# Optimization experiments

Hardware: AMD Instinct MI355X
Metric: run time of the kernel (lower is better)

## Reference

```python
import jax, jax.numpy as jnp
import numpy as np

B, T, U, V = 4, 300, 80, 1024
DE, DD, INNER = 320, 320, 512


def setup_inputs() -> dict:
    key = jax.random.key(0)
    ks = jax.random.split(key, 6)
    enc_state = jax.random.normal(ks[0], (B, T, DE), jnp.float32)
    dec_state = jax.random.normal(ks[1], (B, U + 1, DD), jnp.float32)
    Wf = jax.random.normal(ks[2], (INNER, DE + DD), jnp.float32) / np.float32(np.sqrt(DE + DD))
    bf = jnp.zeros((INNER,), jnp.float32)
    Wp = jax.random.normal(ks[3], (V, INNER), jnp.float32) / np.float32(np.sqrt(INNER))
    bp = jnp.zeros((V,), jnp.float32)
    targets = jax.random.randint(ks[4], (B, U), 1, V).astype(jnp.int32)  # labels avoid blank=0
    inputs_length = jnp.full((B,), T, jnp.int32)
    targets_length = jnp.full((B,), U, jnp.int32)
    return {"enc_state": enc_state, "dec_state": dec_state, "Wf": Wf, "bf": bf,
            "Wp": Wp, "bp": bp, "targets": targets,
            "inputs_length": inputs_length, "targets_length": targets_length}


def joint_logits(enc, dec, Wf, bf, Wp, bp):
    # Linear over concat([enc, dec]) == Linear(enc) + Linear(dec): avoids materializing the concat.
    de = enc.shape[-1]
    Wf_e, Wf_d = Wf[:, :de], Wf[:, de:]
    enc_p = jnp.einsum('btd,id->bti', enc, Wf_e)   # [B,T,inner]
    dec_p = jnp.einsum('bud,id->bui', dec, Wf_d)   # [B,U1,inner]
    h = jnp.tanh(enc_p[:, :, None, :] + dec_p[:, None, :, :] + bf)  # [B,T,U1,inner]
    return jnp.einsum('btui,vi->btuv', h, Wp) + bp  # [B,T,U1,V]


def rnnt_loss(log_probs, targets, t_len, u_len):
    # log_probs: [B,T,U1,V], blank index 0.
    lp_blank = log_probs[..., 0]  # [B,T,U1]
    lp_emit = jnp.take_along_axis(log_probs[:, :, :-1, :], targets[:, None, :, None], axis=3)[..., 0]  # [B,T,U]
    # row0: alpha[0,u] = sum_{k<u} emit[0,k]
    row0 = jnp.pad(jnp.cumsum(lp_emit[:, 0, :], axis=-1), ((0, 0), (1, 0)))  # [B,U1]

    def outer(alpha_prev, xs):
        blank_prev, emit_cur = xs  # [B,U1], [B,U]
        first = alpha_prev[:, 0] + blank_prev[:, 0]  # [B]

        def inner(c, x):
            a_plus_b, e = x  # [B],[B]
            c2 = jnp.logaddexp(a_plus_b, c + e)
            return c2, c2
        xs_in = ((alpha_prev[:, 1:] + blank_prev[:, 1:]).T, emit_cur.T)  # [U,B]
        _, rest = jax.lax.scan(inner, first, xs_in)  # [U,B]
        row = jnp.concatenate([first[None, :], rest], axis=0).T  # [B,U1]
        return row, row

    xs = (jnp.swapaxes(lp_blank[:, :-1, :], 0, 1), jnp.swapaxes(lp_emit[:, 1:, :], 0, 1))
    _, rows = jax.lax.scan(outer, row0, xs)  # [T-1,B,U1]
    alpha = jnp.concatenate([row0[None], rows], axis=0)  # [T,B,U1]
    bidx = jnp.arange(alpha.shape[1])
    ll = alpha[t_len - 1, bidx, u_len] + lp_blank[bidx, t_len - 1, u_len]
    return -jnp.mean(ll)


def reference(enc_state, dec_state, Wf, bf, Wp, bp, targets, inputs_length, targets_length):
    logits = joint_logits(enc_state, dec_state, Wf, bf, Wp, bp).astype(jnp.float32)
    log_probs = jax.nn.log_softmax(logits, axis=-1)
    return rnnt_loss(log_probs, targets, inputs_length, targets_length)
```

## Files before the change

kernel.cpp:

```cpp
#include <hip/hip_runtime.h>

#define B_DIM 4
#define T_DIM 300
#define U_DIM 80
#define UP1   81
#define V_DIM 1024
#define NINNER 512
#define NROWS (B_DIM * T_DIM * UP1)
#define EP_ROWS (B_DIM * T_DIM)
#define DP_ROWS (B_DIM * UP1)
#define NDIAG 380
#define ZSTR  168
#define ZROWS (B_DIM * NDIAG + 8)
#define WF_PART 163840
#define LOG2E 1.44269504088896341f
#define LN2   0.69314718055994531f
#define NEGF  -1e30f

typedef float f32x4 __attribute__((ext_vector_type(4)));
typedef short short8 __attribute__((ext_vector_type(8)));
typedef short short4v __attribute__((ext_vector_type(4)));
typedef __bf16 bf16x8 __attribute__((ext_vector_type(8)));
typedef int int2v __attribute__((ext_vector_type(2)));

static __device__ __forceinline__ short f2bf(float f) {
  return (short)__builtin_bit_cast(unsigned short, (__bf16)f);
}
static __device__ __forceinline__ float bf2f(short s) {
  unsigned int u = ((unsigned int)(unsigned short)s) << 16;
  return __builtin_bit_cast(float, u);
}
static __device__ __forceinline__ float tanh_fast(float x) {
  float e = __builtin_amdgcn_exp2f(x * 2.88539008177792681f);
  return 1.0f - 2.0f * __builtin_amdgcn_rcpf(e + 1.0f);
}
static __device__ __forceinline__ float lse2_2(float a, float b) {
  float mx = fmaxf(a, b), mn = fminf(a, b);
  return mx + __builtin_amdgcn_logf(1.0f + __builtin_amdgcn_exp2f(mn - mx));
}
static __device__ __forceinline__ float ror1f(float x) {
  int r = __builtin_amdgcn_update_dpp(0, __builtin_bit_cast(int, x),
                                      0x13C , 0xF, 0xF, true);
  return __builtin_bit_cast(float, r);
}
static __device__ __forceinline__ float readlanef(float x, int l) {
  return __builtin_bit_cast(float,
      __builtin_amdgcn_readlane(__builtin_bit_cast(int, x), l));
}
static __device__ __forceinline__ f32x4 load4u(const float* p) {
  f32x4 v;
  __builtin_memcpy(&v, p, 16);
  return v;
}
static __device__ __forceinline__ long load8(const void* p) {
  long v;
  __builtin_memcpy(&v, p, 8);
  return v;
}
template <bool HI>
static __device__ __forceinline__ int pkf8(float a, float b, int old) {
  return __builtin_amdgcn_cvt_pk_fp8_f32(a, b, old, HI);
}

#define CVT_NF 81920
#define CVT_NP 131072
#define FILL_N4 ((ZROWS * ZSTR) / 4)
__global__ __launch_bounds__(256) void cvt_kernel(
    const float* __restrict__ Wf, const float* __restrict__ Wp,
    short* __restrict__ WfB, char* __restrict__ WpB8, float* __restrict__ Z) {
  int idx = blockIdx.x * 256 + threadIdx.x;
  if (idx < CVT_NF) {
    float4 v = ((const float4*)Wf)[idx];
    int flat = idx * 4;
    int c = flat / 640;
    int kc = flat - c * 640;
    int part = (kc >= 320);
    int k0 = kc - (part ? 320 : 0);
    int dest = (part ? WF_PART : 0)
             + ((c >> 4) * 10 + (k0 >> 5)) * 512
             + (((k0 >> 3) & 3) * 16 + (c & 15)) * 8 + (k0 & 7);
    short4v o;
    o[0] = f2bf(v.x); o[1] = f2bf(v.y); o[2] = f2bf(v.z); o[3] = f2bf(v.w);
    *(short4v*)(WfB + dest) = o;
  } else if (idx < CVT_NF + CVT_NP) {
    int j = idx - CVT_NF;
    float4 v = ((const float4*)Wp)[j];
    int flat = j * 4;
    int c = flat >> 9;
    int k0 = flat & 511;
    int dest = ((c >> 4) * 16 + (k0 >> 5)) * 512
             + (((k0 >> 3) & 3) * 16 + (c & 15)) * 8 + (k0 & 7);
    int w = pkf8<false>(v.x, v.y, 0);
    w = pkf8<true>(v.z, v.w, w);
    *(int*)(WpB8 + dest) = w;
  } else {
    int i = idx - (CVT_NF + CVT_NP);
    if (i < FILL_N4) ((f32x4*)Z)[i] = (f32x4){NEGF, NEGF, NEGF, NEGF};
  }
}

#define EP_BLOCKS 19
__global__ __launch_bounds__(256) void proj_kernel(
    const float* __restrict__ enc, const float* __restrict__ dec,
    const short* __restrict__ WfB, const float* __restrict__ bfv,
    short* __restrict__ epB, short* __restrict__ dpB) {
  const int half = blockIdx.x & 1;
  const int ob = blockIdx.x >> 1;
  const bool is_dp = (ob >= EP_BLOCKS);
  const int row0 = (is_dp ? ob - EP_BLOCKS : ob) * 64;
  const int nrows = is_dp ? DP_ROWS : EP_ROWS;
  const float* __restrict__ src = is_dp ? dec : enc;
  const short* __restrict__ bb = WfB + (is_dp ? WF_PART : 0);
  short* __restrict__ out = is_dp ? dpB : epB;

  __shared__ short As[64 * 320];
  const int tid = threadIdx.x;

  #pragma unroll
  for (int it = 0; it < 10; ++it) {
    int chunk = it * 256 + tid;
    int m = chunk / 40;
    int c = chunk - m * 40;
    int r = row0 + m;
    short8 hv;
    #pragma unroll
    for (int j = 0; j < 8; ++j) hv[j] = 0;
    if (r < nrows) {
      const float* p = src + (size_t)r * 320 + c * 8;
      float4 a0 = *(const float4*)p;
      float4 a1 = *(const float4*)(p + 4);
      hv[0] = f2bf(a0.x); hv[1] = f2bf(a0.y); hv[2] = f2bf(a0.z); hv[3] = f2bf(a0.w);
      hv[4] = f2bf(a1.x); hv[5] = f2bf(a1.y); hv[6] = f2bf(a1.z); hv[7] = f2bf(a1.w);
    }
    int off = (m * 640 + c * 16) ^ ((m & 7) << 4);
    *(short8*)((char*)As + off) = hv;
  }
  __syncthreads();

  const int lane = tid & 63, wid = tid >> 6;
  const int lr = lane & 15, g = lane >> 4;

  int lin[4], xm[4];
  #pragma unroll
  for (int mf = 0; mf < 4; ++mf) {
    int row = mf * 16 + lr;
    lin[mf] = row * 640 + g * 16;
    xm[mf] = (row & 7) << 4;
  }

  const int n0 = half * 256 + wid * 64;
  const short* bptr[4];
  float bfc[4];
  #pragma unroll
  for (int nf2 = 0; nf2 < 4; ++nf2) {
    bptr[nf2] = bb + (n0 / 16 + nf2) * 5120 + lane * 8;
    bfc[nf2] = is_dp ? bfv[n0 + nf2 * 16 + lr] : 0.f;
  }
  f32x4 acc[4][4];
  #pragma unroll
  for (int mf = 0; mf < 4; ++mf)
    #pragma unroll
    for (int nf2 = 0; nf2 < 4; ++nf2)
      acc[mf][nf2] = (f32x4){0.f, 0.f, 0.f, 0.f};

  #pragma unroll 2
  for (int kk = 0; kk < 10; ++kk) {
    bf16x8 av[4], bv[4];
    #pragma unroll
    for (int mf = 0; mf < 4; ++mf) {
      int off = (lin[mf] + (kk << 6)) ^ xm[mf];
      av[mf] = __builtin_bit_cast(bf16x8, *(const short8*)((const char*)As + off));
    }
    #pragma unroll
    for (int nf2 = 0; nf2 < 4; ++nf2)
      bv[nf2] = __builtin_bit_cast(bf16x8, *(const short8*)(bptr[nf2] + kk * 512));
    #pragma unroll
    for (int mf = 0; mf < 4; ++mf)
      #pragma unroll
      for (int nf2 = 0; nf2 < 4; ++nf2)
        acc[mf][nf2] = __builtin_amdgcn_mfma_f32_16x16x32_bf16(av[mf], bv[nf2], acc[mf][nf2], 0, 0, 0);
  }
  #pragma unroll
  for (int mf = 0; mf < 4; ++mf)
    #pragma unroll
    for (int nf2 = 0; nf2 < 4; ++nf2)
      #pragma unroll
      for (int rr = 0; rr < 4; ++rr) {
        int rowl = mf * 16 + g * 4 + rr;
        int grow = row0 + rowl;
        if (grow < nrows) {
          int col = n0 + nf2 * 16 + lr;
          out[(size_t)grow * NINNER + col] = f2bf(acc[mf][nf2][rr] + bfc[nf2]);
        }
      }
}

#define JROWS 64
__global__ __launch_bounds__(512) void joint_kernel(
    const short* __restrict__ epB, const short* __restrict__ dpB,
    const char* __restrict__ WpB8, const float* __restrict__ bp,
    const int* __restrict__ tgt, float* __restrict__ Z) {
  extern __shared__ char hbuf[];
  __shared__ int ep_off[JROWS], dp_off[JROWS], bld_off[JROWS], eld_off[JROWS], tgt_s[JROWS];
  __shared__ float l0_s[JROWS], lt_s[JROWS];
  __shared__ float ws_s[8][JROWS];

  const int tid = threadIdx.x;
  const int row0 = blockIdx.x * JROWS;

  if (tid < JROWS) {
    int gr = row0 + tid;
    if (gr < NROWS) {
      int b = gr / (T_DIM * UP1);
      int rem = gr - b * (T_DIM * UP1);
      int t = rem / UP1;
      int u = rem - t * UP1;
      ep_off[tid] = (b * T_DIM + t) * NINNER;
      dp_off[tid] = (b * UP1 + u) * NINNER;
      int zrow = (b * NDIAG + (t + u)) * ZSTR;
      bld_off[tid] = zrow + 4 + 2 * u;
      eld_off[tid] = (u < U_DIM) ? (zrow + 4 + 2 * u + 1) : -1;
      tgt_s[tid] = (u < U_DIM) ? tgt[b * U_DIM + u] : 0;
    } else {
      ep_off[tid] = 0; dp_off[tid] = 0; bld_off[tid] = -1; eld_off[tid] = -1; tgt_s[tid] = 0;
    }
    l0_s[tid] = 0.f; lt_s[tid] = 0.f;
  }
  __syncthreads();

  const int m0 = tid >> 4;
  const int m1 = 32 + m0;
  const int cq = tid & 15;
  const short* pe0 = epB + ep_off[m0] + cq * 8;
  const short* pd0 = dpB + dp_off[m0] + cq * 8;
  const short* pe1 = epB + ep_off[m1] + cq * 8;
  const short* pd1 = dpB + dp_off[m1] + cq * 8;
  const int po0 = ((m0 << 9) + (cq << 3)) ^ ((m0 & 7) << 3);
  const int po1 = ((m1 << 9) + (cq << 3)) ^ ((m1 & 7) << 3);

  short8 sev0, sdv0, sev1, sdv1;
#define STAGE_LOAD(q)                                  \
  {                                                    \
    sev0 = *(const short8*)(pe0 + (q) * 128);          \
    sdv0 = *(const short8*)(pd0 + (q) * 128);          \
    sev1 = *(const short8*)(pe1 + (q) * 128);          \
    sdv1 = *(const short8*)(pd1 + (q) * 128);          \
  }
#define STAGE_WRITE(q)                                                    \
  {                                                                       \
    float h0[8], h1[8];                                                   \
    _Pragma("unroll")                                                     \
    for (int j = 0; j < 8; ++j) {                                         \
      h0[j] = tanh_fast(bf2f(sev0[j]) + bf2f(sdv0[j]));                   \
      h1[j] = tanh_fast(bf2f(sev1[j]) + bf2f(sdv1[j]));                   \
    }                                                                     \
    int2v w0, w1;                                                         \
    w0[0] = pkf8<true>(h0[2], h0[3], pkf8<false>(h0[0], h0[1], 0));       \
    w0[1] = pkf8<true>(h0[6], h0[7], pkf8<false>(h0[4], h0[5], 0));       \
    w1[0] = pkf8<true>(h1[2], h1[3], pkf8<false>(h1[0], h1[1], 0));       \
    w1[1] = pkf8<true>(h1[6], h1[7], pkf8<false>(h1[4], h1[5], 0));       \
    *(int2v*)(hbuf + po0 + (q) * 128) = w0;                               \
    *(int2v*)(hbuf + po1 + (q) * 128) = w1;                               \
  }

  STAGE_LOAD(0)
  STAGE_WRITE(0)
  __syncthreads();

  const int lane = tid & 63, wid = tid >> 6;
  const int lr = lane & 15, g = lane >> 4;

  int lin[4];
  #pragma unroll
  for (int mf = 0; mf < 4; ++mf)
    lin[mf] = ((mf * 16 + lr) << 9) + (g << 3);
  const int xm = (lr & 7) << 3;
  int tv[4][4];
  #pragma unroll
  for (int mf = 0; mf < 4; ++mf)
    #pragma unroll
    for (int rr = 0; rr < 4; ++rr)
      tv[mf][rr] = tgt_s[mf * 16 + g * 4 + rr];

  float rsum[4][4];
  #pragma unroll
  for (int mf = 0; mf < 4; ++mf)
    #pragma unroll
    for (int rr = 0; rr < 4; ++rr) rsum[mf][rr] = 0.f;

  #pragma unroll
  for (int sc = 0; sc < 2; ++sc) {
    const int n0 = wid * 128 + sc * 64;
    const char* bptr[4];
    float bpv[4];
    #pragma unroll
    for (int nf = 0; nf < 4; ++nf) {
      bptr[nf] = WpB8 + (n0 / 16 + nf) * 8192 + lane * 8;
      bpv[nf] = bp[n0 + nf * 16 + lr] * LOG2E;
    }
    f32x4 acc[4][4];
    #pragma unroll
    for (int mf = 0; mf < 4; ++mf)
      #pragma unroll
      for (int nf = 0; nf < 4; ++nf)
        acc[mf][nf] = (f32x4){0.f, 0.f, 0.f, 0.f};

    #pragma unroll
    for (int qq = 0; qq < 4; ++qq) {
      if (sc == 0 && qq < 3) STAGE_LOAD(qq + 1)
      #pragma unroll
      for (int i = 0; i < 4; ++i) {
        const int kk = qq * 4 + i;
        long av[4], bv[4];
        #pragma unroll
        for (int mf = 0; mf < 4; ++mf) {
          int off = ((lin[mf] + ((kk & 3) << 5)) ^ xm) + ((kk >> 2) << 7);
          av[mf] = load8(hbuf + off);
        }
        #pragma unroll
        for (int nf = 0; nf < 4; ++nf)
          bv[nf] = load8(bptr[nf] + kk * 512);
        #pragma unroll
        for (int mf = 0; mf < 4; ++mf)
          #pragma unroll
          for (int nf = 0; nf < 4; ++nf)
            acc[mf][nf] = __builtin_amdgcn_mfma_f32_16x16x32_fp8_fp8(av[mf], bv[nf], acc[mf][nf], 0, 0, 0);
      }
      if (sc == 0 && qq < 3) {
        STAGE_WRITE(qq + 1)
        __syncthreads();
      }
    }
    #pragma unroll
    for (int mf = 0; mf < 4; ++mf)
      #pragma unroll
      for (int rr = 0; rr < 4; ++rr) {
        float x0 = __builtin_fmaf(acc[mf][0][rr], LOG2E, bpv[0]);
        float x1 = __builtin_fmaf(acc[mf][1][rr], LOG2E, bpv[1]);
        float x2 = __builtin_fmaf(acc[mf][2][rr], LOG2E, bpv[2]);
        float x3 = __builtin_fmaf(acc[mf][3][rr], LOG2E, bpv[3]);
        int rowl = mf * 16 + g * 4 + rr;
        if (wid == 0 && sc == 0 && lr == 0) l0_s[rowl] = x0;
        int dtv = tv[mf][rr] - n0;
        if (dtv >= 0 && dtv < 64 && (dtv & 15) == lr) {
          int nfi = dtv >> 4;
          lt_s[rowl] = (nfi == 0) ? x0 : (nfi == 1) ? x1 : (nfi == 2) ? x2 : x3;
        }
        rsum[mf][rr] += __builtin_amdgcn_exp2f(x0) + __builtin_amdgcn_exp2f(x1)
                      + __builtin_amdgcn_exp2f(x2) + __builtin_amdgcn_exp2f(x3);
      }
  }
  #pragma unroll
  for (int mf = 0; mf < 4; ++mf)
    #pragma unroll
    for (int rr = 0; rr < 4; ++rr) {
      float s_ = rsum[mf][rr];
      #pragma unroll
      for (int o = 1; o < 16; o <<= 1) s_ += __shfl_xor(s_, o);
      if (lr == 0) ws_s[wid][mf * 16 + g * 4 + rr] = s_;
    }
  __syncthreads();
  if (tid < JROWS) {
    int bo = bld_off[tid];
    if (bo >= 0) {
      float S = 0.f;
      #pragma unroll
      for (int w = 0; w < 8; ++w) S += ws_s[w][tid];
      float lse2v = __builtin_amdgcn_logf(S);
      Z[bo] = l0_s[tid] - lse2v;
      int eo = eld_off[tid];
      if (eo >= 0) Z[eo] = lt_s[tid] - lse2v;
    }
  }
}

#define ACH 8
#define NCH 48
__global__ __launch_bounds__(256) void alpha_kernel(
    const float* __restrict__ Z,
    const int* __restrict__ ilen, const int* __restrict__ ulen_,
    float* __restrict__ out) {
  __shared__ float lls[B_DIM];
  const int tid = threadIdx.x;
  const int b = tid >> 6;
  const int lane = tid & 63;
  const float NEG = NEGF;
  const int tl = ilen[b], ul = ulen_[b];
  const int dstar = tl - 1 + ul;

  const int u0 = lane;
  const int u1 = 64 + lane;
  const bool act1 = (u1 <= 80);
  const int uc1 = act1 ? u1 : 80;

  const float* Zb = Z + (size_t)b * (NDIAG * ZSTR);

  f32x4 Aq0[ACH], Aq1[ACH], Bq0[ACH], Bq1[ACH];

  #define ALOAD(P, c)                                                        \
    {                                                                        \
      const float* base0 = Zb + (c) * (ACH * ZSTR) + 1 + 2 * u0;             \
      const float* base1 = Zb + (c) * (ACH * ZSTR) + 1 + 2 * uc1;            \
      _Pragma("unroll")                                                      \
      for (int j = 0; j < ACH; ++j) {                                        \
        P##q0[j] = load4u(base0 + j * ZSTR);                                 \
        P##q1[j] = load4u(base1 + j * ZSTR);                                 \
      }                                                                      \
    }

  #define ACOMP(P, c)                                                        \
    {                                                                        \
      _Pragma("unroll")                                                      \
      for (int q = 0; q < ACH / 2; ++q) {                                    \
        const int j = 2 * q;                                                 \
        const int s1 = (c) * ACH + j + 1;                                    \
                                    \
        float a63 = readlanef(pa0, 63), a62 = readlanef(pa0, 62);            \
        float s0m1 = ror1f(pa0);                                             \
        float s0m2 = ror1f(s0m1);                                            \
        float s1m1r = ror1f(pa1);                                            \
        float s1m2r = ror1f(s1m1r);                                          \
        float s1m1 = (lane == 0) ? a63 : s1m1r;                              \
        float s1m2 = (lane == 0) ? a62 : ((lane == 1) ? a63 : s1m2r);        \
        float na0, na1;                                                      \
        {                        \
          f32x4 v = P##q0[j], w = P##q0[j + 1];                              \
          float T1 = v[3] + w[3];                                            \
          float T2 = lse2_2(v[2] + w[3], v[1] + w[2]);                       \
          float T3 = v[0] + w[2];                                            \
          float p0 = pa0 + T1;                                               \
          float p1 = s0m1 + T2;                                              \
          float p2 = s0m2 + T3;                                              \
          float mx = fmaxf(fmaxf(p0, p1), p2);                               \
          float ss = __builtin_amdgcn_exp2f(p0 - mx)                         \
                   + __builtin_amdgcn_exp2f(p1 - mx)                         \
                   + __builtin_amdgcn_exp2f(p2 - mx);                        \
          na0 = fmaxf(mx + __builtin_amdgcn_logf(ss), NEG);                  \
        }                                                                    \
        {                                                        \
          f32x4 v = P##q1[j], w = P##q1[j + 1];                              \
          float T1 = v[3] + w[3];                                            \
          float T2 = lse2_2(v[2] + w[3], v[1] + w[2]);                       \
          float T3 = v[0] + w[2];                                            \
          float p0 = pa1 + T1;                                               \
          float p1 = s1m1 + T2;                                              \
          float p2 = s1m2 + T3;                                              \
          float mx = fmaxf(fmaxf(p0, p1), p2);                               \
          float ss = __builtin_amdgcn_exp2f(p0 - mx)                         \
                   + __builtin_amdgcn_exp2f(p1 - mx)                         \
                   + __builtin_amdgcn_exp2f(p2 - mx);                        \
          na1 = fmaxf(mx + __builtin_amdgcn_logf(ss), NEG);                  \
        }                                                                    \
        if (s1 == dstar) {                   \
          float vo0 = lse2_2(pa0 + P##q0[j][3], s0m1 + P##q0[j][2]);         \
          if (u0 == ul) fin = vo0;                                           \
          float vo1 = lse2_2(pa1 + P##q1[j][3], s1m1 + P##q1[j][2]);         \
          if (act1 && u1 == ul) fin = vo1;                                   \
        }                                                                    \
        pa0 = na0; pa1 = na1;                                                \
        if (s1 + 1 == dstar) {              \
          if (u0 == ul) fin = pa0;                                           \
          if (act1 && u1 == ul) fin = pa1;                                   \
        }                                                                    \
      }                                                                      \
    }

  float pa0 = (u0 == 0) ? 0.f : NEG;
  float pa1 = NEG;
  float fin = NEG;
  if (dstar == 0 && u0 == ul) fin = pa0;

  ALOAD(A, 0);
  for (int p = 0; p < NCH / 2; ++p) {
    const int cA = 2 * p, cB = 2 * p + 1;
    ALOAD(B, cB);
    ACOMP(A, cA);
    ALOAD(A, cA + 2);
    ACOMP(B, cB);
  }

  #pragma unroll
  for (int o = 32; o; o >>= 1) fin = fmaxf(fin, __shfl_xor(fin, o));
  if (lane == 0) {
    float last = Zb[(size_t)dstar * ZSTR + 4 + 2 * ul];
    lls[b] = fin + last;
  }
  __syncthreads();
  if (tid == 0)
    out[0] = -(lls[0] + lls[1] + lls[2] + lls[3]) * (LN2 * 0.25f);
}

extern "C" void kernel_launch(void* const* d_in, const int* in_sizes, int n_in,
                              void* d_out, int out_size, void* d_ws, size_t ws_size,
                              hipStream_t stream) {
  const float* enc = (const float*)d_in[0];
  const float* dec = (const float*)d_in[1];
  const float* Wf  = (const float*)d_in[2];
  const float* bfv = (const float*)d_in[3];
  const float* Wp  = (const float*)d_in[4];
  const float* bp  = (const float*)d_in[5];
  const int* targets = (const int*)d_in[6];
  const int* ilen    = (const int*)d_in[7];
  const int* ulen    = (const int*)d_in[8];
  float* out = (float*)d_out;
  char* ws = (char*)d_ws;

  short* WfB  = (short*)(ws + 0);
  char*  WpB8 = (char*)(ws + 655360);
  short* epB  = (short*)(ws + 1179648);
  short* dpB  = (short*)(ws + 2408448);
  float* Z    = (float*)(ws + 2740224);

  cvt_kernel<<<1083, 256, 0, stream>>>(Wf, Wp, WfB, WpB8, Z);
  proj_kernel<<<50, 256, 0, stream>>>(enc, dec, WfB, bfv, epB, dpB);
  joint_kernel<<<(NROWS + JROWS - 1) / JROWS, 512, 32768, stream>>>(epB, dpB, WpB8, bp, targets, Z);
  alpha_kernel<<<1, 256, 0, stream>>>(Z, ilen, ulen, out);
}
```

Before: 186.7 us.

## Split joint into tanh-pack pass and fp8 MFMA GEMM with workspace fallback

Adds a separate kernel that computes tanh(enc_p+dec_p) once per row and stores it as fp8 in an MFMA-fragment-ready layout in workspace. A new joint kernel then streams these fragments directly from global memory with no shared-memory staging and runs the fp8 MFMA GEMM plus the fused log-softmax/gather epilogue. The aim is to take tanh and packing work off the GEMM's critical path and cut LDS use so occupancy rises. In exchange the packed activations (about 50MB) make an extra round trip through global memory, and this path only runs when the workspace is large enough; otherwise the old fused kernel is used.

```diff
diff --git a/kernel.cpp b/kernel.cpp
--- a/kernel.cpp
+++ b/kernel.cpp
@@ -13,6 +13,7 @@
 #define ZSTR  168
 #define ZROWS (B_DIM * NDIAG + 8)
 #define WF_PART 163840
+#define NRG   6080
 #define LOG2E 1.44269504088896341f
 #define LN2   0.69314718055994531f
 #define NEGF  -1e30f
@@ -195,8 +196,158 @@
       }
 }
 
+__global__ __launch_bounds__(256) void hpack_kernel(
+    const short* __restrict__ epB, const short* __restrict__ dpB,
+    char* __restrict__ hpk) {
+  int gt = blockIdx.x * 256 + threadIdx.x;
+  int rg = gt >> 10;
+  int tl = gt & 1023;
+  int kk = tl >> 6;
+  int l = tl & 63;
+  int row = rg * 16 + (l & 15);
+  if (row >= NROWS) row = 0;
+  int b = row / (T_DIM * UP1);
+  int rem = row - b * (T_DIM * UP1);
+  int t = rem / UP1;
+  int u = rem - t * UP1;
+  int k0 = kk * 32 + ((l >> 4) << 3);
+  short8 ev = *(const short8*)(epB + (b * T_DIM + t) * NINNER + k0);
+  short8 dv = *(const short8*)(dpB + (b * UP1 + u) * NINNER + k0);
+  float h[8];
+  #pragma unroll
+  for (int j = 0; j < 8; ++j) h[j] = tanh_fast(bf2f(ev[j]) + bf2f(dv[j]));
+  int2v w;
+  w[0] = pkf8<true>(h[2], h[3], pkf8<false>(h[0], h[1], 0));
+  w[1] = pkf8<true>(h[6], h[7], pkf8<false>(h[4], h[5], 0));
+  *(int2v*)(hpk + (size_t)rg * 8192 + kk * 512 + l * 8) = w;
+}
+
 #define JROWS 64
-__global__ __launch_bounds__(512) void joint_kernel(
+__global__ __launch_bounds__(512) void joint2_kernel(
+    const char* __restrict__ hpk, const char* __restrict__ WpB8,
+    const float* __restrict__ bp, const int* __restrict__ tgt,
+    float* __restrict__ Z) {
+  __shared__ int bld_off[JROWS], eld_off[JROWS], tgt_s[JROWS];
+  __shared__ float l0_s[JROWS], lt_s[JROWS];
+  __shared__ float ws_s[8][JROWS];
+
+  const int tid = threadIdx.x;
+  const int row0 = blockIdx.x * JROWS;
+
+  if (tid < JROWS) {
+    int gr = row0 + tid;
+    if (gr < NROWS) {
+      int b = gr / (T_DIM * UP1);
+      int rem = gr - b * (T_DIM * UP1);
+      int t = rem / UP1;
+      int u = rem - t * UP1;
+      int zrow = (b * NDIAG + (t + u)) * ZSTR;
+      bld_off[tid] = zrow + 4 + 2 * u;
+      eld_off[tid] = (u < U_DIM) ? (zrow + 4 + 2 * u + 1) : -1;
+      tgt_s[tid] = (u < U_DIM) ? tgt[b * U_DIM + u] : 0;
+    } else {
+      bld_off[tid] = -1; eld_off[tid] = -1; tgt_s[tid] = 0;
+    }
+    l0_s[tid] = 0.f; lt_s[tid] = 0.f;
+  }
+  __syncthreads();
+
+  const int lane = tid & 63, wid = tid >> 6;
+  const int lr = lane & 15, g = lane >> 4;
+
+  const char* aptr[4];
+  #pragma unroll
+  for (int mf = 0; mf < 4; ++mf)
+    aptr[mf] = hpk + (size_t)(row0 / 16 + mf) * 8192 + lane * 8;
+  int tv[4][4];
+  #pragma unroll
+  for (int mf = 0; mf < 4; ++mf)
+    #pragma unroll
+    for (int rr = 0; rr < 4; ++rr)
+      tv[mf][rr] = tgt_s[mf * 16 + g * 4 + rr];
+
+  float rsum[4][4];
+  #pragma unroll
+  for (int mf = 0; mf < 4; ++mf)
+    #pragma unroll
+    for (int rr = 0; rr < 4; ++rr) rsum[mf][rr] = 0.f;
+
+  #pragma unroll
+  for (int sc = 0; sc < 2; ++sc) {
+    const int n0 = wid * 128 + sc * 64;
+    const char* bptr[4];
+    float bpv[4];
+    #pragma unroll
+    for (int nf = 0; nf < 4; ++nf) {
+      bptr[nf] = WpB8 + (n0 / 16 + nf) * 8192 + lane * 8;
+      bpv[nf] = bp[n0 + nf * 16 + lr] * LOG2E;
+    }
+    f32x4 acc[4][4];
+    #pragma unroll
+    for (int mf = 0; mf < 4; ++mf)
+      #pragma unroll
+      for (int nf = 0; nf < 4; ++nf)
+        acc[mf][nf] = (f32x4){0.f, 0.f, 0.f, 0.f};
+
+    #pragma unroll 4
+    for (int kk = 0; kk < 16; ++kk) {
+      long av[4], bv[4];
+      #pragma unroll
+      for (int mf = 0; mf < 4; ++mf)
+        av[mf] = load8(aptr[mf] + kk * 512);
+      #pragma unroll
+      for (int nf = 0; nf < 4; ++nf)
+        bv[nf] = load8(bptr[nf] + kk * 512);
+      #pragma unroll
+      for (int mf = 0; mf < 4; ++mf)
+        #pragma unroll
+        for (int nf = 0; nf < 4; ++nf)
+          acc[mf][nf] = __builtin_amdgcn_mfma_f32_16x16x32_fp8_fp8(av[mf], bv[nf], acc[mf][nf], 0, 0, 0);
+    }
+    #pragma unroll
+    for (int mf = 0; mf < 4; ++mf)
+      #pragma unroll
+      for (int rr = 0; rr < 4; ++rr) {
+        float x0 = __builtin_fmaf(acc[mf][0][rr], LOG2E, bpv[0]);
+        float x1 = __builtin_fmaf(acc[mf][1][rr], LOG2E, bpv[1]);
+        float x2 = __builtin_fmaf(acc[mf][2][rr], LOG2E, bpv[2]);
+        float x3 = __builtin_fmaf(acc[mf][3][rr], LOG2E, bpv[3]);
+        int rowl = mf * 16 + g * 4 + rr;
+        if (wid == 0 && sc == 0 && lr == 0) l0_s[rowl] = x0;
+        int dtv = tv[mf][rr] - n0;
+        if (dtv >= 0 && dtv < 64 && (dtv & 15) == lr) {
+          int nfi = dtv >> 4;
+          lt_s[rowl] = (nfi == 0) ? x0 : (nfi == 1) ? x1 : (nfi == 2) ? x2 : x3;
+        }
+        rsum[mf][rr] += __builtin_amdgcn_exp2f(x0) + __builtin_amdgcn_exp2f(x1)
+                      + __builtin_amdgcn_exp2f(x2) + __builtin_amdgcn_exp2f(x3);
+      }
+  }
+  #pragma unroll
+  for (int mf = 0; mf < 4; ++mf)
+    #pragma unroll
+    for (int rr = 0; rr < 4; ++rr) {
+      float s_ = rsum[mf][rr];
+      #pragma unroll
+      for (int o = 1; o < 16; o <<= 1) s_ += __shfl_xor(s_, o);
+      if (lr == 0) ws_s[wid][mf * 16 + g * 4 + rr] = s_;
+    }
+  __syncthreads();
+  if (tid < JROWS) {
+    int bo = bld_off[tid];
+    if (bo >= 0) {
+      float S = 0.f;
+      #pragma unroll
+      for (int w = 0; w < 8; ++w) S += ws_s[w][tid];
+      float lse2v = __builtin_amdgcn_logf(S);
+      Z[bo] = l0_s[tid] - lse2v;
+      int eo = eld_off[tid];
+      if (eo >= 0) Z[eo] = lt_s[tid] - lse2v;
+    }
+  }
+}
+
+__global__ __launch_bounds__(512) void joint_fused_kernel(
     const short* __restrict__ epB, const short* __restrict__ dpB,
     const char* __restrict__ WpB8, const float* __restrict__ bp,
     const int* __restrict__ tgt, float* __restrict__ Z) {
@@ -414,7 +565,6 @@
       for (int q = 0; q < ACH / 2; ++q) {                                    \
         const int j = 2 * q;                                                 \
         const int s1 = (c) * ACH + j + 1;                                    \
-                                    \
         float a63 = readlanef(pa0, 63), a62 = readlanef(pa0, 62);            \
         float s0m1 = ror1f(pa0);                                             \
         float s0m2 = ror1f(s0m1);                                            \
@@ -510,9 +660,17 @@
   short* epB  = (short*)(ws + 1179648);
   short* dpB  = (short*)(ws + 2408448);
   float* Z    = (float*)(ws + 2740224);
+  char*  hpk  = (char*)(ws + 3767040);
+
+  const size_t WS_NEED_SPLIT = 53574400;
 
   cvt_kernel<<<1083, 256, 0, stream>>>(Wf, Wp, WfB, WpB8, Z);
   proj_kernel<<<50, 256, 0, stream>>>(enc, dec, WfB, bfv, epB, dpB);
-  joint_kernel<<<(NROWS + JROWS - 1) / JROWS, 512, 32768, stream>>>(epB, dpB, WpB8, bp, targets, Z);
+  if (ws_size >= WS_NEED_SPLIT) {
+    hpack_kernel<<<NRG * 4, 256, 0, stream>>>(epB, dpB, hpk);
+    joint2_kernel<<<(NROWS + JROWS - 1) / JROWS, 512, 0, stream>>>(hpk, WpB8, bp, targets, Z);
+  } else {
+    joint_fused_kernel<<<(NROWS + JROWS - 1) / JROWS, 512, 32768, stream>>>(epB, dpB, WpB8, bp, targets, Z);
+  }
   alpha_kernel<<<1, 256, 0, stream>>>(Z, ilen, ulen, out);
 }
```

Result: slower. 230.1 us (+23.2%).
